# Kernel optimization log

Hardware: AMD Instinct MI355X
Metric: run time of the kernel (lower is better)

Reference implementation:

```python
import jax, jax.numpy as jnp
import numpy as np

N_NODES = 100000


def _add_self_loops(edge_index, n):
    loop = jnp.arange(n, dtype=edge_index.dtype)
    src = jnp.concatenate([edge_index[0], loop])
    dst = jnp.concatenate([edge_index[1], loop])
    return src, dst


def _gcn_conv(x, src, dst, n, W, b):
    # PyG GCNConv: h = x W; symmetric normalization with self-loops; scatter-add; + bias
    h = x @ W                                   # [N, out]
    ones = jnp.ones(src.shape[0], dtype=x.dtype)
    deg = jax.ops.segment_sum(ones, dst, num_segments=n)   # in-degree incl. self-loop
    dinv = jax.lax.rsqrt(deg)                   # deg >= 1 because of self-loops
    norm = dinv[src] * dinv[dst]                # [E]
    msg = h[src] * norm[:, None]                # gather + scale  [E, out]
    out = jax.ops.segment_sum(msg, dst, num_segments=n)     # scatter-add
    return out + b


def setup_inputs() -> dict:
    key = jax.random.key(0)
    k1, k2, k3, k4, k5 = jax.random.split(key, 5)
    n, e = N_NODES, 1600000
    d_in, d_hid, d_out = 128, 128, 40
    x = jax.random.normal(k1, (n, d_in), dtype=jnp.float32)
    edge_index = jax.random.randint(k2, (2, e), 0, n, dtype=jnp.int32)
    s = 1.0 / np.sqrt(d_in)
    W1 = jax.random.uniform(k3, (d_in, d_hid), jnp.float32, -s, s)
    b1 = jnp.zeros((d_hid,), jnp.float32)
    s2 = 1.0 / np.sqrt(d_hid)
    W2 = jax.random.uniform(k4, (d_hid, d_hid), jnp.float32, -s2, s2)
    b2 = jnp.zeros((d_hid,), jnp.float32)
    Wout = jax.random.uniform(k5, (d_hid, d_out), jnp.float32, -s2, s2)
    bout = jnp.zeros((d_out,), jnp.float32)
    return {"x": x, "edge_index": edge_index, "W1": W1, "b1": b1,
            "W2": W2, "b2": b2, "Wout": Wout, "bout": bout}


def reference(x, edge_index, W1, b1, W2, b2, Wout, bout):
    n = x.shape[0]
    src, dst = _add_self_loops(edge_index, n)
    h = _gcn_conv(x, src, dst, n, W1, b1)
    h = jax.nn.relu(h)
    # dropout(p=0.6) is identity in eval mode
    h = _gcn_conv(h, src, dst, n, W2, b2)
    return h @ Wout + bout
```

## Files before the change

### kernel.cpp

```cpp
#include <hip/hip_runtime.h>


typedef __attribute__((ext_vector_type(8))) short short8;
typedef __attribute__((ext_vector_type(4))) float floatx4;
typedef __attribute__((ext_vector_type(2))) float floatx2;
typedef _Float16 f16;
typedef __attribute__((ext_vector_type(4))) _Float16 half4;

#define CSR_STRIDE 64
#define CH 4096
#define BCAP2 10240

static __device__ inline unsigned short f32_to_bf16(float f) {
    unsigned u = __float_as_uint(f);
    unsigned r = (u + 0x7FFFu + ((u >> 16) & 1u)) >> 16;
    return (unsigned short)r;
}
static __device__ inline float bf16_to_f32(unsigned short h) {
    return __uint_as_float(((unsigned)h) << 16);
}
static __device__ inline void split2(float v, unsigned short& h, unsigned short& l) {
    h = f32_to_bf16(v);
    l = f32_to_bf16(v - bf16_to_f32(h));
}
static __device__ __forceinline__ void fp8x8_acc(floatx2* s2, uint2 v) {
    s2[0] += __builtin_amdgcn_cvt_pk_f32_fp8(v.x, false);
    s2[1] += __builtin_amdgcn_cvt_pk_f32_fp8(v.x, true);
    s2[2] += __builtin_amdgcn_cvt_pk_f32_fp8(v.y, false);
    s2[3] += __builtin_amdgcn_cvt_pk_f32_fp8(v.y, true);
}


__global__ __launch_bounds__(256) void setup1(const float* __restrict__ W2,
                                              const float* __restrict__ Wout,
                                              const float* __restrict__ b2,
                                              const float* __restrict__ bout,
                                              const float* __restrict__ W1,
                                              float* __restrict__ Wc,
                                              float* __restrict__ bc,
                                              unsigned short* __restrict__ wf1,
                                              int* __restrict__ bcur,
                                              unsigned* __restrict__ htz,
                                              unsigned* __restrict__ zz) {
    int tid = blockIdx.x * 256 + threadIdx.x;
    if (tid < 5120) {
        int i = tid / 40, j = tid - (tid / 40) * 40;
        float s = 0.f;
        for (int k = 0; k < 128; k++) s = fmaf(W2[i * 128 + k], Wout[k * 40 + j], s);
        Wc[i * 40 + j] = s;
    } else if (tid < 5160) {
        int j = tid - 5120;
        float s = bout[j];
        for (int k = 0; k < 128; k++) s = fmaf(b2[k], Wout[k * 40 + j], s);
        bc[j] = s;
    } else if (tid < 21544) {
        int e = tid - 5160;
        int k = e >> 7, nn = e & 127;
        int c = nn >> 4, s = k >> 5;
        int lane = (nn & 15) | (((k >> 3) & 3) << 4);
        int j = k & 7;
        int o = ((c * 4 + s) * 64 + lane) * 8 + j;
        wf1[o] = f32_to_bf16(W1[e]);
    } else if (tid < 25640) {
        bcur[tid - 21544] = 0;
    } else if (tid < 25672) {
        htz[tid - 25640] = 0u;
    } else if (tid < 25704) {
        zz[tid - 25672] = 0u;
    }
}


__global__ __launch_bounds__(256) void setup2(const float* __restrict__ Wcf,
                                              unsigned short* __restrict__ wfc) {
    int id = blockIdx.x * 256 + threadIdx.x;
    if (id < 6144) {
        int j = id & 7, lane = (id >> 3) & 63, cs = id >> 9;
        int c = cs >> 2, s = cs & 3;
        int k = s * 32 + ((lane >> 4) & 3) * 8 + j;
        int nn = c * 16 + (lane & 15);
        float v = (nn < 40) ? Wcf[k * 40 + nn] : 0.f;
        unsigned short h, l;
        split2(v, h, l);
        wfc[id] = h;
        wfc[6144 + id] = l;
    }
}


__global__ __launch_bounds__(256) void bin_scatter(const int* __restrict__ src,
                                                   const int* __restrict__ dst,
                                                   int* __restrict__ bcur,
                                                   unsigned* __restrict__ bstore, int e) {
    __shared__ int hist[256];
    __shared__ int gbase[256];
    __shared__ int curs[256];
    int t = threadIdx.x;
    hist[t] = 0;
    __syncthreads();
    int tot4 = e >> 2;
    int base4 = blockIdx.x * (CH / 4);
    unsigned pay[16];
    int cbv[16];
    bool vg[4];
    #pragma unroll
    for (int j = 0; j < 4; j++) {
        int i4 = base4 + t + 256 * j;
        vg[j] = (i4 < tot4);
        if (vg[j]) {
            int4 s4 = ((const int4*)src)[i4];
            int4 d4 = ((const int4*)dst)[i4];
            int dd[4] = {d4.x, d4.y, d4.z, d4.w};
            int ss[4] = {s4.x, s4.y, s4.z, s4.w};
            #pragma unroll
            for (int q = 0; q < 4; q++) {
                int cb = dd[q] >> 9;
                cbv[j * 4 + q] = cb;
                pay[j * 4 + q] = (unsigned)ss[q] | ((unsigned)(dd[q] & 511) << 17);
                atomicAdd(&hist[cb], 1);
            }
        }
    }
    __syncthreads();
    gbase[t] = atomicAdd(&bcur[t * 16], hist[t]);
    curs[t] = 0;
    __syncthreads();
    #pragma unroll
    for (int j = 0; j < 4; j++) {
        if (vg[j]) {
            #pragma unroll
            for (int q = 0; q < 4; q++) {
                int b = cbv[j * 4 + q];
                int pos = atomicAdd(&curs[b], 1);
                int o = gbase[b] + pos;
                if (o < BCAP2) bstore[(size_t)b * BCAP2 + o] = pay[j * 4 + q];
            }
        }
    }
}


__global__ __launch_bounds__(1024) void bin_to_csr(const int* __restrict__ bcur,
                                                   const unsigned* __restrict__ bstore,
                                                   int* __restrict__ csr,
                                                   int* __restrict__ cnt,
                                                   float* __restrict__ dinv, int n) {
    __shared__ int lcur[512];
    int b = blockIdx.x;
    int t = threadIdx.x;
    if (t < 512) lcur[t] = 0;
    __syncthreads();
    int cb = bcur[b * 16];
    if (cb > BCAP2) cb = BCAP2;
    const unsigned* bs = bstore + (size_t)b * BCAP2;
    for (int i = t; i < cb; i += 1024) {
        unsigned v = bs[i];
        int dl = v >> 17;
        int pos = atomicAdd(&lcur[dl], 1);
        if (pos < CSR_STRIDE) {
            int node = (b << 9) | dl;
            csr[(size_t)node * CSR_STRIDE + pos] = (int)(v & 0x1FFFFu);
        }
    }
    __syncthreads();
    if (t < 512) {
        int node = (b << 9) + t;
        if (node < n) {
            int c = min(lcur[t], CSR_STRIDE);
            cnt[node] = c;
            dinv[node] = rsqrtf((float)c + 1.0f);
            int end = (c + 7) & ~7;
            if (end < 8) end = 8;
            size_t base = (size_t)node * CSR_STRIDE;
            for (int k = c; k < end; k++) csr[base + k] = n;
        }
    }
}


__global__ __launch_bounds__(256, 2) void gemm_mfma(const float* __restrict__ A,
                                                    const unsigned short* __restrict__ Wf,
                                                    const float* __restrict__ dinv,
                                                    unsigned char* __restrict__ ht, int M) {
    __shared__ __align__(16) unsigned short Wl[16384];
    {
        const float4* wsrc = (const float4*)Wf;
        float4* wdst = (float4*)Wl;
        #pragma unroll
        for (int i = 0; i < 8; i++) wdst[threadIdx.x + 256 * i] = wsrc[threadIdx.x + 256 * i];
    }
    int wave = threadIdx.x >> 6, lane = threadIdx.x & 63;
    int mlo = lane & 15, kq = lane >> 4;
    int row_base = blockIdx.x * 128 + wave * 32;

    short8 a[2][4];
    #pragma unroll
    for (int rt = 0; rt < 2; rt++) {
        int row = row_base + rt * 16 + mlo;
        if (row > M - 1) row = M - 1;
        const float* pa = A + (size_t)row * 128 + kq * 8;
        #pragma unroll
        for (int s = 0; s < 4; s++) {
            float u[8];
            *(float4*)&u[0] = *(const float4*)(pa + s * 32);
            *(float4*)&u[4] = *(const float4*)(pa + s * 32 + 4);
            short8 ah;
            #pragma unroll
            for (int j = 0; j < 8; j++) ah[j] = (short)f32_to_bf16(u[j]);
            a[rt][s] = ah;
        }
    }
    floatx4 acc[2][8];
    #pragma unroll
    for (int rt = 0; rt < 2; rt++)
        #pragma unroll
        for (int c = 0; c < 8; c++) acc[rt][c] = (floatx4){0.f, 0.f, 0.f, 0.f};
    __syncthreads();

    #pragma unroll
    for (int c = 0; c < 8; c++) {
        #pragma unroll
        for (int s = 0; s < 4; s++) {
            int fo = ((c * 4 + s) * 64 + lane) * 8;
            short8 bhi = *(const short8*)&Wl[fo];
            #pragma unroll
            for (int rt = 0; rt < 2; rt++)
                acc[rt][c] = __builtin_amdgcn_mfma_f32_16x16x32_bf16(a[rt][s], bhi, acc[rt][c], 0, 0, 0);
        }
    }
    #pragma unroll
    for (int rt = 0; rt < 2; rt++) {
        int r0 = row_base + rt * 16 + kq * 4;
        #pragma unroll
        for (int r = 0; r < 4; r++) {
            int row = r0 + r;
            if (row >= M) continue;
            float dd = dinv[row];
            unsigned char* hp = ht + (size_t)row * 128 + mlo;
            #pragma unroll
            for (int c = 0; c < 8; c++) {
                float v = acc[rt][c][r] * dd;
                unsigned pk = __builtin_amdgcn_cvt_pk_fp8_f32(v, v, 0u, false);
                hp[c * 16] = (unsigned char)(pk & 0xFFu);
            }
        }
    }
}


__device__ __forceinline__ void gather16_fp8_to_lds(const unsigned char* __restrict__ ht,
                                                    const int* __restrict__ cnt,
                                                    const int* __restrict__ csr,
                                                    const float* __restrict__ dinv,
                                                    const float* __restrict__ bias,
                                                    int n, unsigned short* __restrict__ ldsA) {
    int g = threadIdx.x >> 4;
    int l = threadIdx.x & 15;
    int d = blockIdx.x * 16 + g;
    if (d >= n) return;
    const unsigned char* hb = ht + l * 8;
    const int4* c4 = (const int4*)(csr + (size_t)d * CSR_STRIDE);
    int4 ea0 = c4[0], ea1 = c4[1];
    int4 eb0 = c4[2], eb1 = c4[3];
    uint2 sv = *(const uint2*)(hb + (size_t)d * 128);
    int len = cnt[d];
    uint2 p0 = *(const uint2*)(hb + (size_t)ea0.x * 128);
    uint2 p1 = *(const uint2*)(hb + (size_t)ea0.y * 128);
    uint2 p2 = *(const uint2*)(hb + (size_t)ea0.z * 128);
    uint2 p3 = *(const uint2*)(hb + (size_t)ea0.w * 128);
    uint2 p4 = *(const uint2*)(hb + (size_t)ea1.x * 128);
    uint2 p5 = *(const uint2*)(hb + (size_t)ea1.y * 128);
    uint2 p6 = *(const uint2*)(hb + (size_t)ea1.z * 128);
    uint2 p7 = *(const uint2*)(hb + (size_t)ea1.w * 128);
    floatx2 s2[4];
    #pragma unroll
    for (int j = 0; j < 4; j++) s2[j] = (floatx2){0.f, 0.f};
    fp8x8_acc(s2, sv);
    int lenp = (len + 7) & ~7;
    if (lenp < 8) lenp = 8;
    for (int it = 8; it < lenp; it += 8) {
        int qidx = (it >> 2) + 2;
        int i0 = qidx > 14 ? 14 : qidx;
        int i1 = qidx + 1 > 15 ? 15 : qidx + 1;
        int4 ec0 = c4[i0];
        int4 ec1 = c4[i1];
        uint2 q0 = *(const uint2*)(hb + (size_t)eb0.x * 128);
        uint2 q1 = *(const uint2*)(hb + (size_t)eb0.y * 128);
        uint2 q2 = *(const uint2*)(hb + (size_t)eb0.z * 128);
        uint2 q3 = *(const uint2*)(hb + (size_t)eb0.w * 128);
        uint2 q4 = *(const uint2*)(hb + (size_t)eb1.x * 128);
        uint2 q5 = *(const uint2*)(hb + (size_t)eb1.y * 128);
        uint2 q6 = *(const uint2*)(hb + (size_t)eb1.z * 128);
        uint2 q7 = *(const uint2*)(hb + (size_t)eb1.w * 128);
        fp8x8_acc(s2, p0); fp8x8_acc(s2, p1); fp8x8_acc(s2, p2); fp8x8_acc(s2, p3);
        fp8x8_acc(s2, p4); fp8x8_acc(s2, p5); fp8x8_acc(s2, p6); fp8x8_acc(s2, p7);
        p0 = q0; p1 = q1; p2 = q2; p3 = q3;
        p4 = q4; p5 = q5; p6 = q6; p7 = q7;
        eb0 = ec0; eb1 = ec1;
    }
    fp8x8_acc(s2, p0); fp8x8_acc(s2, p1); fp8x8_acc(s2, p2); fp8x8_acc(s2, p3);
    fp8x8_acc(s2, p4); fp8x8_acc(s2, p5); fp8x8_acc(s2, p6); fp8x8_acc(s2, p7);
    float dd = dinv[d];
    const float4* b4 = (const float4*)bias;
    float4 ba = b4[l * 2 + 0];
    float4 bq = b4[l * 2 + 1];
    float o[8];
    o[0] = fmaf(s2[0][0], dd, ba.x);
    o[1] = fmaf(s2[0][1], dd, ba.y);
    o[2] = fmaf(s2[1][0], dd, ba.z);
    o[3] = fmaf(s2[1][1], dd, ba.w);
    o[4] = fmaf(s2[2][0], dd, bq.x);
    o[5] = fmaf(s2[2][1], dd, bq.y);
    o[6] = fmaf(s2[3][0], dd, bq.z);
    o[7] = fmaf(s2[3][1], dd, bq.w);
    short8 h8, l8;
    #pragma unroll
    for (int j = 0; j < 8; j++) {
        float v = fmaxf(o[j], 0.f);
        unsigned short sh, sl;
        split2(v, sh, sl);
        h8[j] = (short)sh;
        l8[j] = (short)sl;
    }
    *(short8*)&ldsA[g * 136 + l * 8] = h8;
    *(short8*)&ldsA[2176 + g * 136 + l * 8] = l8;
}

__device__ __forceinline__ void lds_afrag16(const unsigned short* __restrict__ ldsA,
                                            short8 ah[4], short8 al[4]) {
    int lane = threadIdx.x & 63;
    int m = lane & 15, kq = lane >> 4;
    #pragma unroll
    for (int s = 0; s < 4; s++) {
        int c = 4 * s + kq;
        ah[s] = *(const short8*)&ldsA[m * 136 + c * 8];
        al[s] = *(const short8*)&ldsA[2176 + m * 136 + c * 8];
    }
}

__global__ __launch_bounds__(256) void gather_gemm_hidden(const unsigned char* __restrict__ ht,
                                                          const int* __restrict__ cnt,
                                                          const int* __restrict__ csr,
                                                          const float* __restrict__ dinv,
                                                          const float* __restrict__ bias,
                                                          const unsigned short* __restrict__ Wf,
                                                          f16* __restrict__ z, int n) {
    __shared__ __align__(16) unsigned short ldsA[4352];
    gather16_fp8_to_lds(ht, cnt, csr, dinv, bias, n, ldsA);
    __syncthreads();
    int wave = threadIdx.x >> 6, lane = threadIdx.x & 63;
    if (wave == 3) return;
    short8 ah[4], al[4];
    lds_afrag16(ldsA, ah, al);
    int m = lane & 15, kq = lane >> 4;
    int c = wave;
    floatx4 acc = (floatx4){0.f, 0.f, 0.f, 0.f};
    #pragma unroll
    for (int s = 0; s < 4; s++) {
        int fo = ((c * 4 + s) * 64 + lane) * 8;
        short8 bhi = *(const short8*)&Wf[fo];
        short8 blo = *(const short8*)&Wf[6144 + fo];
        acc = __builtin_amdgcn_mfma_f32_16x16x32_bf16(ah[s], bhi, acc, 0, 0, 0);
        acc = __builtin_amdgcn_mfma_f32_16x16x32_bf16(al[s], bhi, acc, 0, 0, 0);
        acc = __builtin_amdgcn_mfma_f32_16x16x32_bf16(ah[s], blo, acc, 0, 0, 0);
    }
    #pragma unroll
    for (int r = 0; r < 4; r++) {
        int row = blockIdx.x * 16 + kq * 4 + r;
        if (row < n) z[(size_t)row * 64 + c * 16 + m] = (f16)(acc[r] * dinv[row]);
    }
}

#define H4ACC(P) { s0 += (float)P[0]; s1 += (float)P[1]; s2 += (float)P[2]; s3 += (float)P[3]; }

__global__ __launch_bounds__(256) void gather_out(const f16* __restrict__ z,
                                                  const int* __restrict__ cnt,
                                                  const int* __restrict__ csr,
                                                  const float* __restrict__ dinv,
                                                  const float* __restrict__ bc,
                                                  float* __restrict__ out, int n) {
    int g = threadIdx.x >> 4;
    int l = threadIdx.x & 15;
    int d = blockIdx.x * 16 + g;
    if (d >= n) return;
    const f16* zb = z + l * 4;
    const int4* c4 = (const int4*)(csr + (size_t)d * CSR_STRIDE);
    int4 ea0 = c4[0], ea1 = c4[1];
    int4 eb0 = c4[2], eb1 = c4[3];
    half4 sv = *(const half4*)(zb + (size_t)d * 64);
    int len = cnt[d];
    half4 p0 = *(const half4*)(zb + (size_t)ea0.x * 64);
    half4 p1 = *(const half4*)(zb + (size_t)ea0.y * 64);
    half4 p2 = *(const half4*)(zb + (size_t)ea0.z * 64);
    half4 p3 = *(const half4*)(zb + (size_t)ea0.w * 64);
    half4 p4 = *(const half4*)(zb + (size_t)ea1.x * 64);
    half4 p5 = *(const half4*)(zb + (size_t)ea1.y * 64);
    half4 p6 = *(const half4*)(zb + (size_t)ea1.z * 64);
    half4 p7 = *(const half4*)(zb + (size_t)ea1.w * 64);
    float s0 = (float)sv[0], s1 = (float)sv[1], s2 = (float)sv[2], s3 = (float)sv[3];
    int lenp = (len + 7) & ~7;
    if (lenp < 8) lenp = 8;
    for (int it = 8; it < lenp; it += 8) {
        int qidx = (it >> 2) + 2;
        int i0 = qidx > 14 ? 14 : qidx;
        int i1 = qidx + 1 > 15 ? 15 : qidx + 1;
        int4 ec0 = c4[i0];
        int4 ec1 = c4[i1];
        half4 q0 = *(const half4*)(zb + (size_t)eb0.x * 64);
        half4 q1 = *(const half4*)(zb + (size_t)eb0.y * 64);
        half4 q2 = *(const half4*)(zb + (size_t)eb0.z * 64);
        half4 q3 = *(const half4*)(zb + (size_t)eb0.w * 64);
        half4 q4 = *(const half4*)(zb + (size_t)eb1.x * 64);
        half4 q5 = *(const half4*)(zb + (size_t)eb1.y * 64);
        half4 q6 = *(const half4*)(zb + (size_t)eb1.z * 64);
        half4 q7 = *(const half4*)(zb + (size_t)eb1.w * 64);
        H4ACC(p0); H4ACC(p1); H4ACC(p2); H4ACC(p3);
        H4ACC(p4); H4ACC(p5); H4ACC(p6); H4ACC(p7);
        p0 = q0; p1 = q1; p2 = q2; p3 = q3;
        p4 = q4; p5 = q5; p6 = q6; p7 = q7;
        eb0 = ec0; eb1 = ec1;
    }
    H4ACC(p0); H4ACC(p1); H4ACC(p2); H4ACC(p3);
    H4ACC(p4); H4ACC(p5); H4ACC(p6); H4ACC(p7);
    if (l < 10) {
        float dd = dinv[d];
        float4 bb = ((const float4*)bc)[l];
        float4 o;
        o.x = fmaf(s0, dd, bb.x);
        o.y = fmaf(s1, dd, bb.y);
        o.z = fmaf(s2, dd, bb.z);
        o.w = fmaf(s3, dd, bb.w);
        *(float4*)(out + (size_t)d * 40 + l * 4) = o;
    }
}

extern "C" void kernel_launch(void* const* d_in, const int* in_sizes, int n_in,
                              void* d_out, int out_size, void* d_ws, size_t ws_size,
                              hipStream_t stream) {
    const float* x    = (const float*)d_in[0];
    const int*   ei   = (const int*)d_in[1];
    const float* W1   = (const float*)d_in[2];
    const float* b1   = (const float*)d_in[3];
    const float* W2   = (const float*)d_in[4];
    const float* b2   = (const float*)d_in[5];
    const float* Wout = (const float*)d_in[6];
    const float* bout = (const float*)d_in[7];

    int N = in_sizes[0] / 128;
    int E = in_sizes[1] / 2;
    const int* srcv = ei;
    const int* dstv = ei + E;

    char* p = (char*)d_ws;
    auto alloc = [&](size_t bytes) { void* r = (void*)p; p += (bytes + 255) & ~(size_t)255; return r; };
    int*      bcur   = (int*)alloc(256 * 16 * 4);
    int*      cnt    = (int*)alloc((size_t)N * 4);
    float*    dinv   = (float*)alloc((size_t)N * 4);
    unsigned* bstore = (unsigned*)alloc((size_t)256 * BCAP2 * 4);
    int*      csr    = (int*)alloc((size_t)N * CSR_STRIDE * 4);
    unsigned short* wf1 = (unsigned short*)alloc(16384 * 2);
    unsigned short* wfc = (unsigned short*)alloc(12288 * 2);
    float*    Wcf    = (float*)alloc(5120 * 4);
    float*    bc     = (float*)alloc(40 * 4);
    unsigned char* ht = (unsigned char*)alloc((size_t)(N + 1) * 128);
    f16*      z      = (f16*)alloc((size_t)(N + 1) * 64 * 2);

    int NB_A  = (E + CH - 1) / CH;
    int NB_B  = (N + 511) >> 9;
    int NB_G  = (N + 127) / 128;
    int NB_GG = (N + 15) / 16;

    setup1<<<101, 256, 0, stream>>>(W2, Wout, b2, bout, W1, Wcf, bc, wf1, bcur,
                                    (unsigned*)(ht + (size_t)N * 128),
                                    (unsigned*)(z + (size_t)N * 64));
    setup2<<<24, 256, 0, stream>>>(Wcf, wfc);

    bin_scatter<<<NB_A, 256, 0, stream>>>(srcv, dstv, bcur, bstore, E);
    bin_to_csr<<<NB_B, 1024, 0, stream>>>(bcur, bstore, csr, cnt, dinv, N);
    gemm_mfma<<<NB_G, 256, 0, stream>>>(x, wf1, dinv, ht, N);

    gather_gemm_hidden<<<NB_GG, 256, 0, stream>>>(ht, cnt, csr, dinv, b1, wfc, z, N);
    gather_out<<<NB_GG, 256, 0, stream>>>(z, cnt, csr, dinv, bc, (float*)d_out, N);
}
```

Before: 217.0 us.

## Sort nodes by padded degree bucket within each block to balance gather work

bin_to_csr now counting-sorts each 512-node group by padded-degree bucket and writes a permutation array. The gather kernels process nodes in that permuted order, so the 16-lane groups and wavefronts in a block handle nodes with similar edge counts. This is meant to reduce divergence in the variable-length gather loop. It costs an extra indirection load per node and scattered writes to z and out. Nodes past N map to node 0 and are recomputed redundantly, which adds a small amount of duplicate work and duplicate writes.

New measurement: 226.7 us. 4.4% more time.

```diff
diff --git a/kernel.cpp b/kernel.cpp
--- a/kernel.cpp
+++ b/kernel.cpp
@@ -144,11 +144,15 @@
                                                    const unsigned* __restrict__ bstore,
                                                    int* __restrict__ csr,
                                                    int* __restrict__ cnt,
-                                                   float* __restrict__ dinv, int n) {
+                                                   float* __restrict__ dinv,
+                                                   int* __restrict__ perm, int n) {
     __shared__ int lcur[512];
+    __shared__ int bhist[8];
+    __shared__ int bbase[8];
     int b = blockIdx.x;
     int t = threadIdx.x;
     if (t < 512) lcur[t] = 0;
+    if (t >= 512 && t < 520) bhist[t - 512] = 0;
     __syncthreads();
     int cb = bcur[b * 16];
     if (cb > BCAP2) cb = BCAP2;
@@ -163,10 +167,12 @@
         }
     }
     __syncthreads();
+    int node = 0, mybkt = 0, mypos = 0;
     if (t < 512) {
-        int node = (b << 9) + t;
+        node = (b << 9) + t;
+        int c = 0;
         if (node < n) {
-            int c = min(lcur[t], CSR_STRIDE);
+            c = min(lcur[t], CSR_STRIDE);
             cnt[node] = c;
             dinv[node] = rsqrtf((float)c + 1.0f);
             int end = (c + 7) & ~7;
@@ -174,6 +180,20 @@
             size_t base = (size_t)node * CSR_STRIDE;
             for (int k = c; k < end; k++) csr[base + k] = n;
         }
+        int lenp8 = (c + 7) >> 3;
+        if (lenp8 < 1) lenp8 = 1;
+        mybkt = lenp8 - 1;
+        mypos = atomicAdd(&bhist[mybkt], 1);
+    }
+    __syncthreads();
+    if (t == 0) {
+        int s = 0;
+        #pragma unroll
+        for (int i = 0; i < 8; i++) { bbase[i] = s; s += bhist[i]; }
+    }
+    __syncthreads();
+    if (t < 512) {
+        perm[(b << 9) + bbase[mybkt] + mypos] = (node < n) ? node : 0;
     }
 }
 
@@ -253,11 +273,11 @@
                                                     const int* __restrict__ csr,
                                                     const float* __restrict__ dinv,
                                                     const float* __restrict__ bias,
+                                                    const int* __restrict__ perm,
                                                     int n, unsigned short* __restrict__ ldsA) {
     int g = threadIdx.x >> 4;
     int l = threadIdx.x & 15;
-    int d = blockIdx.x * 16 + g;
-    if (d >= n) return;
+    int d = perm[blockIdx.x * 16 + g];
     const unsigned char* hb = ht + l * 8;
     const int4* c4 = (const int4*)(csr + (size_t)d * CSR_STRIDE);
     int4 ea0 = c4[0], ea1 = c4[1];
@@ -344,9 +364,10 @@
                                                           const float* __restrict__ dinv,
                                                           const float* __restrict__ bias,
                                                           const unsigned short* __restrict__ Wf,
+                                                          const int* __restrict__ perm,
                                                           f16* __restrict__ z, int n) {
     __shared__ __align__(16) unsigned short ldsA[4352];
-    gather16_fp8_to_lds(ht, cnt, csr, dinv, bias, n, ldsA);
+    gather16_fp8_to_lds(ht, cnt, csr, dinv, bias, perm, n, ldsA);
     __syncthreads();
     int wave = threadIdx.x >> 6, lane = threadIdx.x & 63;
     if (wave == 3) return;
@@ -366,8 +387,8 @@
     }
     #pragma unroll
     for (int r = 0; r < 4; r++) {
-        int row = blockIdx.x * 16 + kq * 4 + r;
-        if (row < n) z[(size_t)row * 64 + c * 16 + m] = (f16)(acc[r] * dinv[row]);
+        int row = perm[blockIdx.x * 16 + kq * 4 + r];
+        z[(size_t)row * 64 + c * 16 + m] = (f16)(acc[r] * dinv[row]);
     }
 }
 
@@ -378,11 +399,11 @@
                                                   const int* __restrict__ csr,
                                                   const float* __restrict__ dinv,
                                                   const float* __restrict__ bc,
+                                                  const int* __restrict__ perm,
                                                   float* __restrict__ out, int n) {
     int g = threadIdx.x >> 4;
     int l = threadIdx.x & 15;
-    int d = blockIdx.x * 16 + g;
-    if (d >= n) return;
+    int d = perm[blockIdx.x * 16 + g];
     const f16* zb = z + l * 4;
     const int4* c4 = (const int4*)(csr + (size_t)d * CSR_STRIDE);
     int4 ea0 = c4[0], ea1 = c4[1];
@@ -465,10 +486,12 @@
     unsigned char* ht = (unsigned char*)alloc((size_t)(N + 1) * 128);
     f16*      z      = (f16*)alloc((size_t)(N + 1) * 64 * 2);
 
+    int NB_B  = (N + 511) >> 9;
+    int*      perm   = (int*)alloc((size_t)NB_B * 512 * 4);
+
     int NB_A  = (E + CH - 1) / CH;
-    int NB_B  = (N + 511) >> 9;
     int NB_G  = (N + 127) / 128;
-    int NB_GG = (N + 15) / 16;
+    int NB_GG = NB_B * 32;
 
     setup1<<<101, 256, 0, stream>>>(W2, Wout, b2, bout, W1, Wcf, bc, wf1, bcur,
                                     (unsigned*)(ht + (size_t)N * 128),
@@ -476,9 +499,9 @@
     setup2<<<24, 256, 0, stream>>>(Wcf, wfc);
 
     bin_scatter<<<NB_A, 256, 0, stream>>>(srcv, dstv, bcur, bstore, E);
-    bin_to_csr<<<NB_B, 1024, 0, stream>>>(bcur, bstore, csr, cnt, dinv, N);
+    bin_to_csr<<<NB_B, 1024, 0, stream>>>(bcur, bstore, csr, cnt, dinv, perm, N);
     gemm_mfma<<<NB_G, 256, 0, stream>>>(x, wf1, dinv, ht, N);
 
-    gather_gemm_hidden<<<NB_GG, 256, 0, stream>>>(ht, cnt, csr, dinv, b1, wfc, z, N);
-    gather_out<<<NB_GG, 256, 0, stream>>>(z, cnt, csr, dinv, bc, (float*)d_out, N);
-}
+    gather_gemm_hidden<<<NB_GG, 256, 0, stream>>>(ht, cnt, csr, dinv, b1, wfc, perm, z, N);
+    gather_out<<<NB_GG, 256, 0, stream>>>(z, cnt, csr, dinv, bc, perm, (float*)d_out, N);
+}
```
